# Optimization experiments

Measured on AMD Instinct MI355X. Metric: run time of the kernel, lower is better.

## Reference

```python
import jax, jax.numpy as jnp
import numpy as np

N, E, Z, H = 16384, 131072, 128, 8
ZH = Z // H
CUTOFF = 5.0


def _dense(key, din, dout, bias=True):
    kw, kb = jax.random.split(key)
    W = (jax.random.normal(kw, (din, dout), jnp.float32) / np.sqrt(din)).astype(jnp.float32)
    if bias:
        return W, jnp.zeros((dout,), jnp.float32)
    return W


def setup_inputs() -> dict:
    key = jax.random.key(0)
    ks = jax.random.split(key, 24)
    edge_index = jax.random.randint(ks[0], (2, E), 0, N)
    h_N_1_Z = jax.random.normal(ks[1], (N, 1, Z), jnp.float32)
    mu_N_L2_Z = jax.random.normal(ks[2], (N, 3, Z), jnp.float32) * 0.1
    ev = jax.random.normal(ks[3], (E, 3), jnp.float32)
    edge_vec_E_3 = ev / jnp.linalg.norm(ev, axis=-1, keepdims=True)
    edge_emb_E_Z = jax.random.normal(ks[4], (E, Z), jnp.float32)
    edge_weight_E = jax.random.uniform(ks[5], (E,), jnp.float32, 0.5, CUTOFF)
    deg = jax.ops.segment_sum(jnp.ones((E,), jnp.float32), edge_index[1], num_segments=N)
    num_edges_expanded_E = deg[edge_index[1]]
    inp = dict(edge_index=edge_index, h_N_1_Z=h_N_1_Z, mu_N_L2_Z=mu_N_L2_Z,
               edge_vec_E_3=edge_vec_E_3, edge_emb_E_Z=edge_emb_E_Z,
               edge_weight_E=edge_weight_E, num_edges_expanded_E=num_edges_expanded_E)
    inp['W_q'], inp['b_q'] = _dense(ks[6], Z, Z)
    inp['W_k'], inp['b_k'] = _dense(ks[7], Z, Z)
    inp['W_gs1'], inp['b_gs1'] = _dense(ks[8], Z, Z)
    inp['W_gs2'], inp['b_gs2'] = _dense(ks[9], Z, 3 * Z)
    inp['W_gv1'], inp['b_gv1'] = _dense(ks[10], Z, Z)
    inp['W_gv2'], inp['b_gv2'] = _dense(ks[11], Z, 3 * Z)
    inp['W_phik'], inp['b_phik'] = _dense(ks[12], Z, Z)
    inp['W_re'], inp['b_re'] = _dense(ks[13], Z, 3 * Z)
    inp['W_vq'] = _dense(ks[14], Z, Z, bias=False)   # vecq_w, no bias
    inp['W_vk0'] = _dense(ks[15], Z, Z, bias=False)  # veck_w[0] (lmax=1), no bias
    inp['W_lin'], inp['b_lin'] = _dense(ks[16], Z, Z)  # lin_w_linear
    inp['W_eu1'], inp['b_eu1'] = _dense(ks[17], Z, Z)  # edge_attr_up MLP [Z,Z,Z]
    inp['W_eu2'], inp['b_eu2'] = _dense(ks[18], Z, Z)
    return inp


def reference(edge_index, h_N_1_Z, mu_N_L2_Z, edge_vec_E_3, edge_emb_E_Z,
              edge_weight_E, num_edges_expanded_E,
              W_q, b_q, W_k, b_k, W_gs1, b_gs1, W_gs2, b_gs2,
              W_gv1, b_gv1, W_gv2, b_gv2, W_phik, b_phik, W_re, b_re,
              W_vq, W_vk0, W_lin, b_lin, W_eu1, b_eu1, W_eu2, b_eu2):
    silu = jax.nn.silu
    src, dst = edge_index[0], edge_index[1]  # messages j->i aggregated at dst=i
    hs = h_N_1_Z[:, 0]                        # (N, Z); layernorm='' -> identity
    q = (hs @ W_q + b_q).reshape(N, H, ZH)
    k = (hs @ W_k + b_k).reshape(N, H, ZH)
    x3 = silu(hs @ W_gs1 + b_gs1) @ W_gs2 + b_gs2    # gamma_s: (N, 3Z)
    val3 = silu(hs @ W_gv1 + b_gv1) @ W_gv2 + b_gv2  # gamma_v: (N, 3Z)
    r_attn = silu(edge_emb_E_Z @ W_phik + b_phik).reshape(E, H, ZH)
    r_ij = edge_emb_E_Z @ W_re + b_re                # (E, 3Z)

    # per-edge multi-head attention with segment softmax over target node
    logits = jnp.sum(q[dst] * k[src] * r_attn, axis=-1)        # (E, H)
    m = jax.ops.segment_max(logits, dst, num_segments=N)
    ex = jnp.exp(logits - m[dst])
    den = jax.ops.segment_sum(ex, dst, num_segments=N)
    attn = ex / den[dst]
    attn = attn * (jnp.sqrt(num_edges_expanded_E)[:, None] / np.float32(np.sqrt(Z)))

    sea = (attn[..., None] * val3[src].reshape(E, H, 3 * ZH)).reshape(E, 3 * Z)
    cut = 0.5 * (jnp.cos(jnp.pi * edge_weight_E / CUTOFF) + 1.0) * (edge_weight_E < CUTOFF)
    x_ij = cut[:, None] * sea * (x3[src] * r_ij)               # (E, 3Z)
    o_s, o_d, o_t = x_ij[:, :Z], x_ij[:, Z:2 * Z], x_ij[:, 2 * Z:]
    dmu_ij = o_d[:, None, :] * edge_vec_E_3[..., None] + o_t[:, None, :] * mu_N_L2_Z[src]  # (E,3,Z)

    h_out = h_N_1_Z + jax.ops.segment_sum(o_s, dst, num_segments=N)[:, None, :]
    mu_out = mu_N_L2_Z + jax.ops.segment_sum(dmu_ij, dst, num_segments=N)

    # edge update (sep_vecj, lmax=1 -> single degree block)
    w1 = jnp.einsum('nlz,ze->nle', mu_out, W_vq)
    w2 = jnp.einsum('nlz,ze->nle', mu_out, W_vk0)
    w1_d = jnp.sum(w1[dst] * edge_vec_E_3[..., None], axis=1)  # (E, evec)
    w2_d = jnp.sum(w2[src] * edge_vec_E_3[..., None], axis=1)
    w_dot = jnp.tanh((w1_d * w2_d) @ W_lin + b_lin)            # gated='gatedt'
    f_up = silu(edge_emb_E_Z @ W_eu1 + b_eu1) @ W_eu2 + b_eu2  # edge_attr_up MLP
    df_ij = edge_emb_E_Z + f_up * w_dot
    return h_out, mu_out, df_ij
```

## Files before the change

kernel.cpp:

```cpp
#include <hip/hip_runtime.h>
#include <math.h>

#define NN 16384
#define EE 131072
#define ZZ 128
#define HH 8

typedef short bf16x8 __attribute__((ext_vector_type(8)));
typedef float f32x4 __attribute__((ext_vector_type(4)));
typedef unsigned short ushort4v __attribute__((ext_vector_type(4)));
typedef unsigned short ushort8v __attribute__((ext_vector_type(8)));

__device__ __forceinline__ float silu_f(float x) { return x / (1.0f + __expf(-x)); }

__device__ __forceinline__ unsigned short f2bf(float x) {
    unsigned u = __float_as_uint(x);
    unsigned r = (u >> 16) & 1u;
    u += 0x7fffu + r;
    return (unsigned short)(u >> 16);
}
__device__ __forceinline__ float bf2f(unsigned short x) {
    return __uint_as_float(((unsigned)x) << 16);
}

__device__ __forceinline__ f32x4 mfma16(bf16x8 a, bf16x8 b, f32x4 c) {
    return __builtin_amdgcn_mfma_f32_16x16x32_bf16(a, b, c, 0, 0, 0);
}

__device__ __forceinline__ void stageB(const unsigned short* Wt, char* lB, int t) {
    const uint4* Wg = (const uint4*)Wt;
#pragma unroll
    for (int i = 0; i < 8; ++i) {
        const int cid = t + i * 256;
        const int n = cid >> 4, c16 = cid & 15;
        *(uint4*)(lB + ((n * 256 + c16 * 16) ^ ((n & 7) << 4))) = Wg[cid];
    }
}

struct WPrep {
    const float* w[13];
    int P[13];
    int tile0[14];
};

__global__ __launch_bounds__(128) void prep_weights(WPrep wp, unsigned short* wt) {
    int b = blockIdx.x, wi = 0;
    while (b >= wp.tile0[wi + 1]) ++wi;
    const int cg = (b - wp.tile0[wi]) * 128;
    const float* w = wp.w[wi];
    unsigned short* o = wt + (size_t)wp.tile0[wi] * 16384;
    const int P = wp.P[wi];
    const int t = threadIdx.x;
    for (int k0 = 0; k0 < 128; k0 += 8) {
        ushort8v v;
#pragma unroll
        for (int j = 0; j < 8; ++j) v[j] = f2bf(w[(size_t)(k0 + j) * P + cg + t]);
        *(ushort8v*)(o + (size_t)(cg + t) * 128 + k0) = v;
    }
}

struct BPrep {
    const float* b[13];
    int off[14];
};

__global__ __launch_bounds__(256) void prep_bias(BPrep bp, float* bcat) {
    const int idx = blockIdx.x * 256 + threadIdx.x;
    if (idx >= 2432) return;
    int wi = 0;
    while (idx >= bp.off[wi + 1]) ++wi;
    bcat[idx] = bp.b[wi] ? bp.b[wi][idx - bp.off[wi]] : 0.f;
}

__global__ __launch_bounds__(256) void prep_mub(const float* __restrict__ mu,
                                                unsigned short* __restrict__ mub) {
    const size_t idx = (size_t)blockIdx.x * 256 + threadIdx.x;
    const float4 a = ((const float4*)mu)[idx * 2];
    const float4 b = ((const float4*)mu)[idx * 2 + 1];
    ushort8v v;
    v[0] = f2bf(a.x); v[1] = f2bf(a.y); v[2] = f2bf(a.z); v[3] = f2bf(a.w);
    v[4] = f2bf(b.x); v[5] = f2bf(b.y); v[6] = f2bf(b.z); v[7] = f2bf(b.w);
    *(ushort8v*)(mub + idx * 8) = v;
}

template <int ACT, int INBF, int DUMP, int GATHERA>
__global__ __launch_bounds__(256, 2) void mm_bf16(
    const void* __restrict__ Av, const unsigned short* __restrict__ Wt,
    const float* __restrict__ bias, unsigned short* __restrict__ C,
    const unsigned short* __restrict__ aux, unsigned short* __restrict__ dumpA,
    const int* __restrict__ rowmap, int P, int As)
{
    __shared__ uint4 lA4[2048];
    __shared__ uint4 lB4[2048];
    char* lA = (char*)lA4;
    char* lB = (char*)lB4;
    const int t = threadIdx.x;
    const size_t row0 = (size_t)blockIdx.x * 128;
    const int cg = blockIdx.y * 128;
    if (INBF) {
        const uint4* Ag = (const uint4*)((const unsigned short*)Av + row0 * As);
        const int rs = As >> 3;
#pragma unroll
        for (int i = 0; i < 8; ++i) {
            const int chunk = t + i * 256;
            const int r = chunk >> 4, c16 = chunk & 15;
            *(uint4*)(lA + ((r * 256 + c16 * 16) ^ ((r & 7) << 4))) = Ag[r * rs + c16];
        }
    } else {
#pragma unroll
        for (int i = 0; i < 16; ++i) {
            const int f4 = t + i * 256;
            const int r = f4 >> 5, c4 = f4 & 31;
            const size_t gr = GATHERA ? (size_t)rowmap[row0 + r] : row0 + r;
            const float4 v = ((const float4*)((const float*)Av + gr * As))[c4];
            ushort4v bb;
            bb.x = f2bf(v.x); bb.y = f2bf(v.y); bb.z = f2bf(v.z); bb.w = f2bf(v.w);
            *(ushort4v*)(lA + ((r * 256 + c4 * 8) ^ ((r & 7) << 4))) = bb;
        }
    }
    stageB(Wt + (size_t)cg * 128, lB, t);
    __syncthreads();
    if (DUMP) {
#pragma unroll
        for (int i = 0; i < 8; ++i) {
            const int ch = t + i * 256;
            const int row = ch >> 4, cpos = ch & 15;
            const uint4 v = *(const uint4*)(lA + ((row * 256 + cpos * 16) ^ ((row & 7) << 4)));
            *(uint4*)(dumpA + (row0 + row) * 128 + cpos * 8) = v;
        }
    }
    const int lane = t & 63, wid = t >> 6;
    const int rbase = (wid >> 1) * 64, cbase = (wid & 1) * 64;
    const int lr = lane & 15, lgp = lane >> 4;
    f32x4 acc[4][4];
#pragma unroll
    for (int i = 0; i < 4; ++i)
#pragma unroll
        for (int j = 0; j < 4; ++j) acc[i][j] = (f32x4){0.f, 0.f, 0.f, 0.f};
#pragma unroll
    for (int ks = 0; ks < 4; ++ks) {
        bf16x8 av[4], bv[4];
#pragma unroll
        for (int mt = 0; mt < 4; ++mt) {
            const int r = rbase + mt * 16 + lr;
            av[mt] = *(const bf16x8*)(lA + ((r * 256 + ks * 64 + lgp * 16) ^ ((r & 7) << 4)));
        }
#pragma unroll
        for (int nt = 0; nt < 4; ++nt) {
            const int c = cbase + nt * 16 + lr;
            bv[nt] = *(const bf16x8*)(lB + ((c * 256 + ks * 64 + lgp * 16) ^ ((c & 7) << 4)));
        }
#pragma unroll
        for (int mt = 0; mt < 4; ++mt)
#pragma unroll
            for (int nt = 0; nt < 4; ++nt)
                acc[mt][nt] = mfma16(av[mt], bv[nt], acc[mt][nt]);
    }
    __syncthreads();
#pragma unroll
    for (int nt = 0; nt < 4; ++nt) {
        const int col = cbase + nt * 16 + lr;
        const int gcol = cg + col;
        const float b = bias[gcol];
#pragma unroll
        for (int mt = 0; mt < 4; ++mt) {
#pragma unroll
            for (int j = 0; j < 4; ++j) {
                const int row = rbase + mt * 16 + lgp * 4 + j;
                float v = acc[mt][nt][j] + b;
                if (ACT == 1) v = silu_f(v);
                if (ACT == 2) v = v * bf2f(aux[(row0 + row) * (size_t)P + gcol]);
                *(unsigned short*)(lB + ((row * 256 + col * 2) ^ ((row & 7) << 4))) = f2bf(v);
            }
        }
    }
    __syncthreads();
#pragma unroll
    for (int i = 0; i < 8; ++i) {
        const int ch = t + i * 256;
        const int row = ch >> 4, cpos = ch & 15;
        const uint4 v = *(const uint4*)(lB + ((row * 256 + cpos * 16) ^ ((row & 7) << 4)));
        *(uint4*)(C + (row0 + row) * (size_t)P + cg + cpos * 8) = v;
    }
}

__global__ __launch_bounds__(256, 3) void edge_mlp(
    const float* __restrict__ emb, const int* __restrict__ perm,
    const unsigned short* __restrict__ Wt1, const float* __restrict__ b1,
    const unsigned short* __restrict__ Wt2, const float* __restrict__ b2,
    unsigned short* __restrict__ embp, unsigned short* __restrict__ fup)
{
    __shared__ uint4 lA4[2048];
    char* lA = (char*)lA4;
    const int t = threadIdx.x;
    const size_t e0 = (size_t)blockIdx.x * 128;
#pragma unroll
    for (int i = 0; i < 16; ++i) {
        const int f4 = t + i * 256;
        const int r = f4 >> 5, c4 = f4 & 31;
        const size_t gr = (size_t)perm[e0 + r];
        const float4 v = ((const float4*)(emb + gr * 128))[c4];
        ushort4v bb;
        bb.x = f2bf(v.x); bb.y = f2bf(v.y); bb.z = f2bf(v.z); bb.w = f2bf(v.w);
        *(ushort4v*)(lA + ((r * 256 + c4 * 8) ^ ((r & 7) << 4))) = bb;
    }
    __syncthreads();
#pragma unroll
    for (int i = 0; i < 8; ++i) {
        const int ch = t + i * 256;
        const int row = ch >> 4, cpos = ch & 15;
        const uint4 v = *(const uint4*)(lA + ((row * 256 + cpos * 16) ^ ((row & 7) << 4)));
        *(uint4*)(embp + (e0 + row) * 128 + cpos * 8) = v;
    }
    const int lane = t & 63, wid = t >> 6;
    const int rbase = (wid >> 1) * 64, cbase = (wid & 1) * 64;
    const int lr = lane & 15, lgp = lane >> 4;
    f32x4 acc[4][4];
#pragma unroll
    for (int i = 0; i < 4; ++i)
#pragma unroll
        for (int j = 0; j < 4; ++j) acc[i][j] = (f32x4){0.f, 0.f, 0.f, 0.f};
#pragma unroll
    for (int ks = 0; ks < 4; ++ks) {
        bf16x8 av[4], bv[4];
#pragma unroll
        for (int mt = 0; mt < 4; ++mt) {
            const int r = rbase + mt * 16 + lr;
            av[mt] = *(const bf16x8*)(lA + ((r * 256 + ks * 64 + lgp * 16) ^ ((r & 7) << 4)));
        }
#pragma unroll
        for (int nt = 0; nt < 4; ++nt)
            bv[nt] = *(const bf16x8*)(Wt1 + (size_t)(cbase + nt * 16 + lr) * 128 + ks * 32 + lgp * 8);
#pragma unroll
        for (int mt = 0; mt < 4; ++mt)
#pragma unroll
            for (int nt = 0; nt < 4; ++nt)
                acc[mt][nt] = mfma16(bv[nt], av[mt], acc[mt][nt]);
    }
    __syncthreads();
#pragma unroll
    for (int mt = 0; mt < 4; ++mt) {
        const int row = rbase + mt * 16 + lr;
#pragma unroll
        for (int nt = 0; nt < 4; ++nt) {
            const int col = cbase + nt * 16 + lgp * 4;
            const float4 b4 = *(const float4*)(b1 + col);
            ushort4v st;
            st.x = f2bf(silu_f(acc[mt][nt][0] + b4.x));
            st.y = f2bf(silu_f(acc[mt][nt][1] + b4.y));
            st.z = f2bf(silu_f(acc[mt][nt][2] + b4.z));
            st.w = f2bf(silu_f(acc[mt][nt][3] + b4.w));
            *(ushort4v*)(lA + ((row * 256 + col * 2) ^ ((row & 7) << 4))) = st;
        }
    }
    __syncthreads();
#pragma unroll
    for (int i = 0; i < 4; ++i)
#pragma unroll
        for (int j = 0; j < 4; ++j) acc[i][j] = (f32x4){0.f, 0.f, 0.f, 0.f};
#pragma unroll
    for (int ks = 0; ks < 4; ++ks) {
        bf16x8 av[4], bv[4];
#pragma unroll
        for (int mt = 0; mt < 4; ++mt) {
            const int r = rbase + mt * 16 + lr;
            av[mt] = *(const bf16x8*)(lA + ((r * 256 + ks * 64 + lgp * 16) ^ ((r & 7) << 4)));
        }
#pragma unroll
        for (int nt = 0; nt < 4; ++nt)
            bv[nt] = *(const bf16x8*)(Wt2 + (size_t)(cbase + nt * 16 + lr) * 128 + ks * 32 + lgp * 8);
#pragma unroll
        for (int mt = 0; mt < 4; ++mt)
#pragma unroll
            for (int nt = 0; nt < 4; ++nt)
                acc[mt][nt] = mfma16(bv[nt], av[mt], acc[mt][nt]);
    }
    __syncthreads();
#pragma unroll
    for (int mt = 0; mt < 4; ++mt) {
        const int row = rbase + mt * 16 + lr;
#pragma unroll
        for (int nt = 0; nt < 4; ++nt) {
            const int col = cbase + nt * 16 + lgp * 4;
            const float4 b4 = *(const float4*)(b2 + col);
            ushort4v st;
            st.x = f2bf(acc[mt][nt][0] + b4.x);
            st.y = f2bf(acc[mt][nt][1] + b4.y);
            st.z = f2bf(acc[mt][nt][2] + b4.z);
            st.w = f2bf(acc[mt][nt][3] + b4.w);
            *(ushort4v*)(lA + ((row * 256 + col * 2) ^ ((row & 7) << 4))) = st;
        }
    }
    __syncthreads();
#pragma unroll
    for (int i = 0; i < 8; ++i) {
        const int ch = t + i * 256;
        const int row = ch >> 4, cpos = ch & 15;
        const uint4 v = *(const uint4*)(lA + ((row * 256 + cpos * 16) ^ ((row & 7) << 4)));
        *(uint4*)(fup + (e0 + row) * 128 + cpos * 8) = v;
    }
}

__global__ __launch_bounds__(256) void attn_kernel(
    const int* __restrict__ row_start, const int* __restrict__ srcp,
    const unsigned short* __restrict__ qkb, const unsigned short* __restrict__ rabp,
    const float* __restrict__ ewp, float* __restrict__ attnw)
{
    const int t = threadIdx.x;
    const int n = blockIdx.x * 4 + (t >> 6);
    const int lane = t & 63;
    const int el = lane >> 3, h = lane & 7;
    const int beg = row_start[n], end = row_start[n + 1];
    if (beg == end) return;
    const ushort8v q0 = *(const ushort8v*)(qkb + (size_t)n * 256 + h * 16);
    const ushort8v q1 = *(const ushort8v*)(qkb + (size_t)n * 256 + h * 16 + 8);
    float m = -1e30f, den = 0.f;
    for (int i0 = beg; i0 < end; i0 += 8) {
        const int i = i0 + el;
        const bool valid = i < end;
        const int ii = valid ? i : beg;
        const int s = srcp[ii];
        const ushort8v k0 = *(const ushort8v*)(qkb + (size_t)s * 256 + 128 + h * 16);
        const ushort8v k1 = *(const ushort8v*)(qkb + (size_t)s * 256 + 128 + h * 16 + 8);
        const ushort8v r0 = *(const ushort8v*)(rabp + (size_t)ii * 128 + h * 16);
        const ushort8v r1 = *(const ushort8v*)(rabp + (size_t)ii * 128 + h * 16 + 8);
        float lgv = 0.f;
#pragma unroll
        for (int j = 0; j < 8; ++j) lgv += bf2f(q0[j]) * bf2f(k0[j]) * bf2f(r0[j]);
#pragma unroll
        for (int j = 0; j < 8; ++j) lgv += bf2f(q1[j]) * bf2f(k1[j]) * bf2f(r1[j]);
        if (!valid) lgv = -1e30f;
        else attnw[(size_t)i * 8 + h] = lgv;
        float cm = lgv;
        cm = fmaxf(cm, __shfl_xor(cm, 8));
        cm = fmaxf(cm, __shfl_xor(cm, 16));
        cm = fmaxf(cm, __shfl_xor(cm, 32));
        const float nm = fmaxf(m, cm);
        float ex = valid ? __expf(lgv - nm) : 0.f;
        float cd = ex;
        cd += __shfl_xor(cd, 8);
        cd += __shfl_xor(cd, 16);
        cd += __shfl_xor(cd, 32);
        den = den * __expf(m - nm) + cd;
        m = nm;
    }
    const float sc = sqrtf((float)(end - beg)) * 0.08838834764831845f / den;
    for (int i0 = beg; i0 < end; i0 += 8) {
        const int i = i0 + el;
        if (i >= end) continue;
        const float w = ewp[i];
        const float cut = (w < 5.0f) ? 0.5f * (cosf(w * 0.62831853071795864f) + 1.0f) : 0.0f;
        const float lgv = attnw[(size_t)i * 8 + h];
        attnw[(size_t)i * 8 + h] = __expf(lgv - m) * sc * cut;
    }
}

__global__ __launch_bounds__(256, 3) void combine_mfma(
    const unsigned short* __restrict__ embp, const unsigned short* __restrict__ Wt_re,
    const float* __restrict__ bre, const float* __restrict__ attnw,
    unsigned short* __restrict__ ob)
{
    __shared__ uint4 lA4[2048];
    __shared__ float attnS[128 * 8];
    __shared__ uint4 scr4[512];
    char* lA = (char*)lA4;
    const int t = threadIdx.x;
    const size_t e0 = (size_t)blockIdx.x * 128;
    {
        const uint4* Ag = (const uint4*)(embp + e0 * 128);
#pragma unroll
        for (int i = 0; i < 8; ++i) {
            const int chunk = t + i * 256;
            const int r = chunk >> 4, c16 = chunk & 15;
            *(uint4*)(lA + ((r * 256 + c16 * 16) ^ ((r & 7) << 4))) = Ag[chunk];
        }
    }
    ((float4*)attnS)[t] = ((const float4*)(attnw + e0 * 8))[t];
    __syncthreads();
    const int lane = t & 63, wid = t >> 6;
    const int rbase = (wid >> 1) * 64, cbase = (wid & 1) * 64;
    const int lr = lane & 15, lgp = lane >> 4;
    char* swr = (char*)scr4 + wid * 2048;
    const int r2 = lane >> 3, c16r = lane & 7;
    for (int cg3 = 0; cg3 < 3; ++cg3) {
        const unsigned short* Wp = Wt_re + (size_t)cg3 * 16384;
        f32x4 acc[4][4];
#pragma unroll
        for (int i = 0; i < 4; ++i)
#pragma unroll
            for (int j = 0; j < 4; ++j) acc[i][j] = (f32x4){0.f, 0.f, 0.f, 0.f};
#pragma unroll
        for (int ks = 0; ks < 4; ++ks) {
            bf16x8 av[4], bv[4];
#pragma unroll
            for (int mt = 0; mt < 4; ++mt) {
                const int r = rbase + mt * 16 + lr;
                av[mt] = *(const bf16x8*)(lA + ((r * 256 + ks * 64 + lgp * 16) ^ ((r & 7) << 4)));
            }
#pragma unroll
            for (int nt = 0; nt < 4; ++nt)
                bv[nt] = *(const bf16x8*)(Wp + (size_t)(cbase + nt * 16 + lr) * 128 + ks * 32 + lgp * 8);
#pragma unroll
            for (int mt = 0; mt < 4; ++mt)
#pragma unroll
                for (int nt = 0; nt < 4; ++nt)
                    acc[mt][nt] = mfma16(bv[nt], av[mt], acc[mt][nt]);
        }
        const int cgo = cg3 * 128;
#pragma unroll
        for (int mt = 0; mt < 4; ++mt) {
            const int row = rbase + mt * 16 + lr;
            const float* aS = attnS + row * 8;
#pragma unroll
            for (int nt = 0; nt < 4; ++nt) {
                const int wc = nt * 16 + lgp * 4;
                const int gcol = cgo + cbase + wc;
                const float coef = aS[gcol / 48];
                const float4 b4 = *(const float4*)(bre + gcol);
                ushort4v st;
                st.x = f2bf((acc[mt][nt][0] + b4.x) * coef);
                st.y = f2bf((acc[mt][nt][1] + b4.y) * coef);
                st.z = f2bf((acc[mt][nt][2] + b4.z) * coef);
                st.w = f2bf((acc[mt][nt][3] + b4.w) * coef);
                *(ushort4v*)(swr + ((lr * 128 + wc * 2) ^ ((lr & 7) << 4))) = st;
            }
#pragma unroll
            for (int i = 0; i < 2; ++i) {
                const int rr = r2 + i * 8;
                const uint4 v = *(const uint4*)(swr + ((rr * 128 + c16r * 16) ^ ((rr & 7) << 4)));
                const size_t row_g = e0 + rbase + mt * 16 + rr;
                *(uint4*)(ob + row_g * 384 + cgo + cbase + c16r * 8) = v;
            }
        }
    }
}

__global__ __launch_bounds__(256, 3) void wdot_fused(
    const unsigned short* __restrict__ w12, const int* __restrict__ srcp,
    const int* __restrict__ dstp, const float* __restrict__ evp,
    const unsigned short* __restrict__ Wt_lin, const float* __restrict__ bl,
    const unsigned short* __restrict__ embp, const unsigned short* __restrict__ fup,
    const int* __restrict__ perm, float* __restrict__ df)
{
    __shared__ uint4 lA4[2048];
    char* lA = (char*)lA4;
    const int t = threadIdx.x;
    const size_t e0 = (size_t)blockIdx.x * 128;
#pragma unroll
    for (int i = 0; i < 8; ++i) {
        const int chunk = t + i * 256;
        const int r = chunk >> 4, c8 = chunk & 15;
        const size_t slot = e0 + r;
        const int s = srcp[slot], d = dstp[slot];
        const float e0v = evp[slot * 3 + 0], e1v = evp[slot * 3 + 1], e2v = evp[slot * 3 + 2];
        const ushort8v a0 = *(const ushort8v*)(w12 + ((size_t)d * 3 + 0) * 256 + c8 * 8);
        const ushort8v a1 = *(const ushort8v*)(w12 + ((size_t)d * 3 + 1) * 256 + c8 * 8);
        const ushort8v a2 = *(const ushort8v*)(w12 + ((size_t)d * 3 + 2) * 256 + c8 * 8);
        const ushort8v c0 = *(const ushort8v*)(w12 + ((size_t)s * 3 + 0) * 256 + 128 + c8 * 8);
        const ushort8v c1 = *(const ushort8v*)(w12 + ((size_t)s * 3 + 1) * 256 + 128 + c8 * 8);
        const ushort8v c2 = *(const ushort8v*)(w12 + ((size_t)s * 3 + 2) * 256 + 128 + c8 * 8);
        ushort8v o;
#pragma unroll
        for (int j = 0; j < 8; ++j) {
            const float av = e0v * bf2f(a0[j]) + e1v * bf2f(a1[j]) + e2v * bf2f(a2[j]);
            const float bv = e0v * bf2f(c0[j]) + e1v * bf2f(c1[j]) + e2v * bf2f(c2[j]);
            o[j] = f2bf(av * bv);
        }
        *(ushort8v*)(lA + ((r * 256 + c8 * 16) ^ ((r & 7) << 4))) = o;
    }
    __syncthreads();
    const int lane = t & 63, wid = t >> 6;
    const int rbase = (wid >> 1) * 64, cbase = (wid & 1) * 64;
    const int lr = lane & 15, lgp = lane >> 4;
    f32x4 acc[4][4];
#pragma unroll
    for (int i = 0; i < 4; ++i)
#pragma unroll
        for (int j = 0; j < 4; ++j) acc[i][j] = (f32x4){0.f, 0.f, 0.f, 0.f};
#pragma unroll
    for (int ks = 0; ks < 4; ++ks) {
        bf16x8 av[4], bv[4];
#pragma unroll
        for (int mt = 0; mt < 4; ++mt) {
            const int r = rbase + mt * 16 + lr;
            av[mt] = *(const bf16x8*)(lA + ((r * 256 + ks * 64 + lgp * 16) ^ ((r & 7) << 4)));
        }
#pragma unroll
        for (int nt = 0; nt < 4; ++nt)
            bv[nt] = *(const bf16x8*)(Wt_lin + (size_t)(cbase + nt * 16 + lr) * 128 + ks * 32 + lgp * 8);
#pragma unroll
        for (int mt = 0; mt < 4; ++mt)
#pragma unroll
            for (int nt = 0; nt < 4; ++nt)
                acc[mt][nt] = mfma16(bv[nt], av[mt], acc[mt][nt]);
    }
    __syncthreads();
    char* swr = lA + wid * 8192;
    const int r2 = lane >> 2, c4 = lane & 3;
#pragma unroll
    for (int mt = 0; mt < 4; ++mt) {
#pragma unroll
        for (int nt = 0; nt < 4; ++nt) {
            const int wc = nt * 16 + lgp * 4;
            const float4 b4 = *(const float4*)(bl + cbase + wc);
            float4 v;
            v.x = tanhf(acc[mt][nt][0] + b4.x);
            v.y = tanhf(acc[mt][nt][1] + b4.y);
            v.z = tanhf(acc[mt][nt][2] + b4.z);
            v.w = tanhf(acc[mt][nt][3] + b4.w);
            *(float4*)(swr + ((lr * 256 + wc * 4) ^ ((lr & 7) << 4))) = v;
        }
#pragma unroll
        for (int i = 0; i < 4; ++i) {
            const int chunk = i * 4 + c4;
            const float4 v = *(const float4*)(swr + ((r2 * 256 + chunk * 16) ^ ((r2 & 7) << 4)));
            const int row = rbase + mt * 16 + r2;
            const size_t sbase = (e0 + row) * 128 + cbase + chunk * 4;
            const ushort4v em = *(const ushort4v*)(embp + sbase);
            const ushort4v fu = *(const ushort4v*)(fup + sbase);
            const size_t orow = (size_t)perm[e0 + row];
            float4 o;
            o.x = bf2f(em.x) + bf2f(fu.x) * v.x;
            o.y = bf2f(em.y) + bf2f(fu.y) * v.y;
            o.z = bf2f(em.z) + bf2f(fu.z) * v.z;
            o.w = bf2f(em.w) + bf2f(fu.w) * v.w;
            *(float4*)(df + orow * 128 + cbase + chunk * 4) = o;
        }
    }
}

__global__ __launch_bounds__(256) void hist_kernel(const int* __restrict__ dst, int* __restrict__ counts) {
    const int e = blockIdx.x * 256 + threadIdx.x;
    atomicAdd(&counts[dst[e]], 1);
}

__global__ __launch_bounds__(256) void scan_kernel(const int* __restrict__ counts,
                                                   int* __restrict__ row_start,
                                                   int* __restrict__ cursor) {
    __shared__ int part[256];
    const int t = threadIdx.x;
    const int base = t * 64;
    int local[64];
    int s = 0;
#pragma unroll
    for (int i = 0; i < 64; ++i) { local[i] = s; s += counts[base + i]; }
    part[t] = s;
    __syncthreads();
    for (int off = 1; off < 256; off <<= 1) {
        int v = (t >= off) ? part[t - off] : 0;
        __syncthreads();
        part[t] += v;
        __syncthreads();
    }
    const int prev = (t == 0) ? 0 : part[t - 1];
#pragma unroll
    for (int i = 0; i < 64; ++i) {
        const int v = prev + local[i];
        row_start[base + i] = v;
        cursor[base + i] = v;
    }
    if (t == 255) row_start[NN] = prev + s;
}

__global__ __launch_bounds__(256) void fill_kernel(
    const int* __restrict__ src, const int* __restrict__ dst,
    const float* __restrict__ ewt, const float* __restrict__ ev,
    int* __restrict__ cursor, int* __restrict__ perm, int* __restrict__ srcp,
    int* __restrict__ dstp, float* __restrict__ ewp, float* __restrict__ evp)
{
    const int e = blockIdx.x * 256 + threadIdx.x;
    const int d = dst[e];
    const int p = atomicAdd(&cursor[d], 1);
    perm[p] = e;
    srcp[p] = src[e];
    dstp[p] = d;
    ewp[p] = ewt[e];
    evp[p * 3 + 0] = ev[e * 3 + 0];
    evp[p * 3 + 1] = ev[e * 3 + 1];
    evp[p * 3 + 2] = ev[e * 3 + 2];
}

__global__ __launch_bounds__(256) void gather_kernel(
    const int* __restrict__ row_start, const int* __restrict__ srcp,
    const unsigned short* __restrict__ ob, const unsigned short* __restrict__ xv,
    const unsigned short* __restrict__ mub, const float* __restrict__ evp,
    const float* __restrict__ h_in, const float* __restrict__ mu_in,
    float* __restrict__ h_out, float* __restrict__ mu_out)
{
    const int n = blockIdx.x * 4 + (threadIdx.x >> 6);
    const int t2 = (threadIdx.x & 63) * 2;
    const int beg = row_start[n], end = row_start[n + 1];
    float2 h2 = *(const float2*)(h_in + (size_t)n * 128 + t2);
    float2 m0 = *(const float2*)(mu_in + (size_t)n * 384 + t2);
    float2 m1 = *(const float2*)(mu_in + (size_t)n * 384 + 128 + t2);
    float2 m2 = *(const float2*)(mu_in + (size_t)n * 384 + 256 + t2);
#define GSTEP(i)  { \
        const int s = srcp[i]; \
        const float ev0 = evp[(i) * 3 + 0], ev1 = evp[(i) * 3 + 1], ev2 = evp[(i) * 3 + 2]; \
        const unsigned op0 = *(const unsigned*)(ob + (size_t)(i) * 384 + t2); \
        const unsigned op1 = *(const unsigned*)(ob + (size_t)(i) * 384 + 128 + t2); \
        const unsigned op2 = *(const unsigned*)(ob + (size_t)(i) * 384 + 256 + t2); \
        const unsigned xp0 = *(const unsigned*)(xv + (size_t)s * 384 + t2); \
        const unsigned xp1 = *(const unsigned*)(xv + (size_t)s * 384 + 128 + t2); \
        const unsigned xp2 = *(const unsigned*)(xv + (size_t)s * 384 + 256 + t2); \
        const unsigned mp0 = *(const unsigned*)(mub + (size_t)s * 384 + t2); \
        const unsigned mp1 = *(const unsigned*)(mub + (size_t)s * 384 + 128 + t2); \
        const unsigned mp2 = *(const unsigned*)(mub + (size_t)s * 384 + 256 + t2); \
        const float os0 = bf2f((unsigned short)op0) * bf2f((unsigned short)xp0); \
        const float os1 = bf2f((unsigned short)(op0 >> 16)) * bf2f((unsigned short)(xp0 >> 16)); \
        const float od0 = bf2f((unsigned short)op1) * bf2f((unsigned short)xp1); \
        const float od1 = bf2f((unsigned short)(op1 >> 16)) * bf2f((unsigned short)(xp1 >> 16)); \
        const float ot0 = bf2f((unsigned short)op2) * bf2f((unsigned short)xp2); \
        const float ot1 = bf2f((unsigned short)(op2 >> 16)) * bf2f((unsigned short)(xp2 >> 16)); \
        h2.x += os0; h2.y += os1; \
        m0.x += od0 * ev0 + ot0 * bf2f((unsigned short)mp0); \
        m0.y += od1 * ev0 + ot1 * bf2f((unsigned short)(mp0 >> 16)); \
        m1.x += od0 * ev1 + ot0 * bf2f((unsigned short)mp1); \
        m1.y += od1 * ev1 + ot1 * bf2f((unsigned short)(mp1 >> 16)); \
        m2.x += od0 * ev2 + ot0 * bf2f((unsigned short)mp2); \
        m2.y += od1 * ev2 + ot1 * bf2f((unsigned short)(mp2 >> 16)); \
    }
    int i = beg;
    for (; i + 1 < end; i += 2) { GSTEP(i); GSTEP(i + 1); }
    if (i < end) GSTEP(i);
#undef GSTEP
    *(float2*)(h_out + (size_t)n * 128 + t2) = h2;
    *(float2*)(mu_out + (size_t)n * 384 + t2) = m0;
    *(float2*)(mu_out + (size_t)n * 384 + 128 + t2) = m1;
    *(float2*)(mu_out + (size_t)n * 384 + 256 + t2) = m2;
}

extern "C" void kernel_launch(void* const* d_in, const int* in_sizes, int n_in,
                              void* d_out, int out_size, void* d_ws, size_t ws_size,
                              hipStream_t stream) {
    const int* eidx = (const int*)d_in[0];
    const int* src = eidx;
    const int* dst = eidx + EE;
    const float* h_in  = (const float*)d_in[1];
    const float* mu_in = (const float*)d_in[2];
    const float* ev    = (const float*)d_in[3];
    const float* emb   = (const float*)d_in[4];
    const float* ewt   = (const float*)d_in[5];
    const float* W_q   = (const float*)d_in[7];  const float* b_q   = (const float*)d_in[8];
    const float* W_k   = (const float*)d_in[9];  const float* b_k   = (const float*)d_in[10];
    const float* W_gs1 = (const float*)d_in[11]; const float* b_gs1 = (const float*)d_in[12];
    const float* W_gs2 = (const float*)d_in[13]; const float* b_gs2 = (const float*)d_in[14];
    const float* W_gv1 = (const float*)d_in[15]; const float* b_gv1 = (const float*)d_in[16];
    const float* W_gv2 = (const float*)d_in[17]; const float* b_gv2 = (const float*)d_in[18];
    const float* W_phik= (const float*)d_in[19]; const float* b_phik= (const float*)d_in[20];
    const float* W_re  = (const float*)d_in[21]; const float* b_re  = (const float*)d_in[22];
    const float* W_vq  = (const float*)d_in[23];
    const float* W_vk0 = (const float*)d_in[24];
    const float* W_lin = (const float*)d_in[25]; const float* b_lin = (const float*)d_in[26];
    const float* W_eu1 = (const float*)d_in[27]; const float* b_eu1 = (const float*)d_in[28];
    const float* W_eu2 = (const float*)d_in[29]; const float* b_eu2 = (const float*)d_in[30];

    float* out    = (float*)d_out;
    float* h_out  = out;
    float* mu_out = out + (size_t)NN * ZZ;
    float* df     = out + (size_t)NN * ZZ * 4;

    const size_t NZ = (size_t)NN * ZZ, N3Z = (size_t)NN * 3 * ZZ, EZ = (size_t)EE * ZZ;
    const size_t EH = (size_t)EE * HH;
    char* p = (char*)d_ws;
    unsigned short* qkb   = (unsigned short*)p; p += NZ * 2 * 2;
    unsigned short* tmpn2 = (unsigned short*)p; p += NZ * 2 * 2;
    unsigned short* x3b   = (unsigned short*)p; p += N3Z * 2;
    unsigned short* xv    = (unsigned short*)p; p += N3Z * 2;
    unsigned short* mub   = (unsigned short*)p; p += N3Z * 2;
    unsigned short* w12   = (unsigned short*)p; p += N3Z * 2 * 2;
    unsigned short* embp  = (unsigned short*)p; p += EZ * 2;
    unsigned short* rabp  = (unsigned short*)p; p += EZ * 2;
    unsigned short* fup   = (unsigned short*)p; p += EZ * 2;
    unsigned short* ob    = (unsigned short*)p; p += EZ * 3 * 2;
    float* attnw          = (float*)p;          p += EH * 4;
    unsigned short* wt    = (unsigned short*)p; p += 2432 * 128 * 2;
    float* bcat           = (float*)p;          p += 2432 * 4;
    int* counts           = (int*)p;            p += NN * 4;
    int* cursor           = (int*)p;            p += NN * 4;
    int* row_start        = (int*)p;            p += (NN + 1) * 4;
    int* perm             = (int*)p;            p += EE * 4;
    int* srcp             = (int*)p;            p += EE * 4;
    int* dstp             = (int*)p;            p += EE * 4;
    float* ewp            = (float*)p;          p += EE * 4;
    float* evp            = (float*)p;          p += EE * 12;

    const float* wsrc[13] = {W_q, W_k, W_gs1, W_gv1, W_gs2, W_gv2, W_phik,
                             W_re, W_vq, W_vk0, W_lin, W_eu1, W_eu2};
    const float* bsrc[13] = {b_q, b_k, b_gs1, b_gv1, b_gs2, b_gv2, b_phik,
                             b_re, nullptr, nullptr, b_lin, b_eu1, b_eu2};
    const int Ps[13] = {128, 128, 128, 128, 384, 384, 128, 384, 128, 128, 128, 128, 128};
    WPrep wp; BPrep bp;
    int tiles = 0;
    for (int i = 0; i < 13; ++i) {
        wp.w[i] = wsrc[i]; wp.P[i] = Ps[i]; wp.tile0[i] = tiles;
        bp.b[i] = bsrc[i]; bp.off[i] = tiles * 128;
        tiles += Ps[i] / 128;
    }
    wp.tile0[13] = tiles; bp.off[13] = tiles * 128;
    unsigned short* wT[13]; const float* bC[13];
    for (int i = 0; i < 13; ++i) { wT[i] = wt + (size_t)wp.tile0[i] * 16384; bC[i] = bcat + bp.off[i]; }

    dim3 blk(256);
    prep_weights<<<dim3(tiles), dim3(128), 0, stream>>>(wp, wt);
    prep_bias<<<dim3(10), blk, 0, stream>>>(bp, bcat);
    prep_mub<<<dim3(N3Z / 8 / 256), blk, 0, stream>>>(mu_in, mub);
    hipMemsetAsync(counts, 0, NN * 4, stream);
    hist_kernel<<<dim3(EE/256), blk, 0, stream>>>(dst, counts);
    scan_kernel<<<dim3(1), blk, 0, stream>>>(counts, row_start, cursor);
    fill_kernel<<<dim3(EE/256), blk, 0, stream>>>(src, dst, ewt, ev, cursor, perm, srcp, dstp, ewp, evp);
    mm_bf16<0,0,0,0><<<dim3(NN/128, 2), blk, 0, stream>>>(h_in, wT[0], bC[0], qkb, nullptr, nullptr, nullptr, 256, 128);
    mm_bf16<1,0,0,0><<<dim3(NN/128, 2), blk, 0, stream>>>(h_in, wT[2], bC[2], tmpn2, nullptr, nullptr, nullptr, 256, 128);
    mm_bf16<0,1,0,0><<<dim3(NN/128, 3), blk, 0, stream>>>(tmpn2, wT[4], bC[4], x3b, nullptr, nullptr, nullptr, 384, 256);
    mm_bf16<2,1,0,0><<<dim3(NN/128, 3), blk, 0, stream>>>(tmpn2 + 128, wT[5], bC[5], xv, x3b, nullptr, nullptr, 384, 256);
    edge_mlp<<<dim3(EE/128), blk, 0, stream>>>(emb, perm, wT[11], bC[11], wT[12], bC[12], embp, fup);
    mm_bf16<1,1,0,0><<<dim3(EE/128, 1), blk, 0, stream>>>(embp, wT[6], bC[6], rabp, nullptr, nullptr, nullptr, 128, 128);
    attn_kernel<<<dim3(NN/4), blk, 0, stream>>>(row_start, srcp, qkb, rabp, ewp, attnw);
    combine_mfma<<<dim3(EE/128), blk, 0, stream>>>(embp, wT[7], bC[7], attnw, ob);
    gather_kernel<<<dim3(NN/4), blk, 0, stream>>>(
        row_start, srcp, ob, xv, mub, evp, h_in, mu_in, h_out, mu_out);
    mm_bf16<0,0,0,0><<<dim3(3*NN/128, 2), blk, 0, stream>>>(mu_out, wT[8], bC[8], w12, nullptr, nullptr, nullptr, 256, 128);
    wdot_fused<<<dim3(EE/128), blk, 0, stream>>>(
        w12, srcp, dstp, evp, wT[10], bC[10], embp, fup, perm, df);
}
```

Measured before the change: 386.6 us.

## Fuse phik edge GEMM into edge_mlp and read embp directly in combine

The separate mm_bf16 launch that computed silu(emb@W_phik+b) into rabp is folded into edge_mlp, reusing the emb tile already in LDS. Epilogues in edge_mlp now stage each warp's 16-row slab through a small per-warp scratch, which drops block-wide barriers. combine_mfma no longer stages embp into LDS and loads A fragments straight from global memory, and its occupancy hint is raised from 3 to 5. The goal is to save one kernel launch, one read of embp and some LDS and sync overhead. The cost is more per-block work in edge_mlp and uncoalesced global A loads in combine.

```diff
diff --git a/kernel.cpp b/kernel.cpp
--- a/kernel.cpp
+++ b/kernel.cpp
@@ -186,11 +186,14 @@
 
 __global__ __launch_bounds__(256, 3) void edge_mlp(
     const float* __restrict__ emb, const int* __restrict__ perm,
+    const unsigned short* __restrict__ Wt_phik, const float* __restrict__ b_phik,
     const unsigned short* __restrict__ Wt1, const float* __restrict__ b1,
     const unsigned short* __restrict__ Wt2, const float* __restrict__ b2,
-    unsigned short* __restrict__ embp, unsigned short* __restrict__ fup)
+    unsigned short* __restrict__ embp, unsigned short* __restrict__ rabp,
+    unsigned short* __restrict__ fup)
 {
     __shared__ uint4 lA4[2048];
+    __shared__ uint4 scr4[512];
     char* lA = (char*)lA4;
     const int t = threadIdx.x;
     const size_t e0 = (size_t)blockIdx.x * 128;
@@ -215,7 +218,51 @@
     const int lane = t & 63, wid = t >> 6;
     const int rbase = (wid >> 1) * 64, cbase = (wid & 1) * 64;
     const int lr = lane & 15, lgp = lane >> 4;
+    char* swr = (char*)scr4 + wid * 2048;
+    const int r2 = lane >> 3, c16r = lane & 7;
     f32x4 acc[4][4];
+#pragma unroll
+    for (int i = 0; i < 4; ++i)
+#pragma unroll
+        for (int j = 0; j < 4; ++j) acc[i][j] = (f32x4){0.f, 0.f, 0.f, 0.f};
+#pragma unroll
+    for (int ks = 0; ks < 4; ++ks) {
+        bf16x8 av[4], bv[4];
+#pragma unroll
+        for (int mt = 0; mt < 4; ++mt) {
+            const int r = rbase + mt * 16 + lr;
+            av[mt] = *(const bf16x8*)(lA + ((r * 256 + ks * 64 + lgp * 16) ^ ((r & 7) << 4)));
+        }
+#pragma unroll
+        for (int nt = 0; nt < 4; ++nt)
+            bv[nt] = *(const bf16x8*)(Wt_phik + (size_t)(cbase + nt * 16 + lr) * 128 + ks * 32 + lgp * 8);
+#pragma unroll
+        for (int mt = 0; mt < 4; ++mt)
+#pragma unroll
+            for (int nt = 0; nt < 4; ++nt)
+                acc[mt][nt] = mfma16(bv[nt], av[mt], acc[mt][nt]);
+    }
+#pragma unroll
+    for (int mt = 0; mt < 4; ++mt) {
+#pragma unroll
+        for (int nt = 0; nt < 4; ++nt) {
+            const int wc = nt * 16 + lgp * 4;
+            const float4 b4 = *(const float4*)(b_phik + cbase + wc);
+            ushort4v st;
+            st.x = f2bf(silu_f(acc[mt][nt][0] + b4.x));
+            st.y = f2bf(silu_f(acc[mt][nt][1] + b4.y));
+            st.z = f2bf(silu_f(acc[mt][nt][2] + b4.z));
+            st.w = f2bf(silu_f(acc[mt][nt][3] + b4.w));
+            *(ushort4v*)(swr + ((lr * 128 + wc * 2) ^ ((lr & 7) << 4))) = st;
+        }
+#pragma unroll
+        for (int i = 0; i < 2; ++i) {
+            const int rr = r2 + i * 8;
+            const uint4 v = *(const uint4*)(swr + ((rr * 128 + c16r * 16) ^ ((rr & 7) << 4)));
+            const size_t row_g = e0 + rbase + mt * 16 + rr;
+            *(uint4*)(rabp + row_g * 128 + cbase + c16r * 8) = v;
+        }
+    }
 #pragma unroll
     for (int i = 0; i < 4; ++i)
 #pragma unroll
@@ -275,29 +322,26 @@
             for (int nt = 0; nt < 4; ++nt)
                 acc[mt][nt] = mfma16(bv[nt], av[mt], acc[mt][nt]);
     }
-    __syncthreads();
 #pragma unroll
     for (int mt = 0; mt < 4; ++mt) {
-        const int row = rbase + mt * 16 + lr;
 #pragma unroll
         for (int nt = 0; nt < 4; ++nt) {
-            const int col = cbase + nt * 16 + lgp * 4;
-            const float4 b4 = *(const float4*)(b2 + col);
+            const int wc = nt * 16 + lgp * 4;
+            const float4 b4 = *(const float4*)(b2 + cbase + wc);
             ushort4v st;
             st.x = f2bf(acc[mt][nt][0] + b4.x);
             st.y = f2bf(acc[mt][nt][1] + b4.y);
             st.z = f2bf(acc[mt][nt][2] + b4.z);
             st.w = f2bf(acc[mt][nt][3] + b4.w);
-            *(ushort4v*)(lA + ((row * 256 + col * 2) ^ ((row & 7) << 4))) = st;
-        }
-    }
-    __syncthreads();
-#pragma unroll
-    for (int i = 0; i < 8; ++i) {
-        const int ch = t + i * 256;
-        const int row = ch >> 4, cpos = ch & 15;
-        const uint4 v = *(const uint4*)(lA + ((row * 256 + cpos * 16) ^ ((row & 7) << 4)));
-        *(uint4*)(fup + (e0 + row) * 128 + cpos * 8) = v;
+            *(ushort4v*)(swr + ((lr * 128 + wc * 2) ^ ((lr & 7) << 4))) = st;
+        }
+#pragma unroll
+        for (int i = 0; i < 2; ++i) {
+            const int rr = r2 + i * 8;
+            const uint4 v = *(const uint4*)(swr + ((rr * 128 + c16r * 16) ^ ((rr & 7) << 4)));
+            const size_t row_g = e0 + rbase + mt * 16 + rr;
+            *(uint4*)(fup + row_g * 128 + cbase + c16r * 8) = v;
+        }
     }
 }
 
@@ -355,26 +399,15 @@
     }
 }
 
-__global__ __launch_bounds__(256, 3) void combine_mfma(
+__global__ __launch_bounds__(256, 5) void combine_mfma(
     const unsigned short* __restrict__ embp, const unsigned short* __restrict__ Wt_re,
     const float* __restrict__ bre, const float* __restrict__ attnw,
     unsigned short* __restrict__ ob)
 {
-    __shared__ uint4 lA4[2048];
     __shared__ float attnS[128 * 8];
     __shared__ uint4 scr4[512];
-    char* lA = (char*)lA4;
     const int t = threadIdx.x;
     const size_t e0 = (size_t)blockIdx.x * 128;
-    {
-        const uint4* Ag = (const uint4*)(embp + e0 * 128);
-#pragma unroll
-        for (int i = 0; i < 8; ++i) {
-            const int chunk = t + i * 256;
-            const int r = chunk >> 4, c16 = chunk & 15;
-            *(uint4*)(lA + ((r * 256 + c16 * 16) ^ ((r & 7) << 4))) = Ag[chunk];
-        }
-    }
     ((float4*)attnS)[t] = ((const float4*)(attnw + e0 * 8))[t];
     __syncthreads();
     const int lane = t & 63, wid = t >> 6;
@@ -393,10 +426,8 @@
         for (int ks = 0; ks < 4; ++ks) {
             bf16x8 av[4], bv[4];
 #pragma unroll
-            for (int mt = 0; mt < 4; ++mt) {
-                const int r = rbase + mt * 16 + lr;
-                av[mt] = *(const bf16x8*)(lA + ((r * 256 + ks * 64 + lgp * 16) ^ ((r & 7) << 4)));
-            }
+            for (int mt = 0; mt < 4; ++mt)
+                av[mt] = *(const bf16x8*)(embp + (e0 + rbase + mt * 16 + lr) * 128 + ks * 32 + lgp * 8);
 #pragma unroll
             for (int nt = 0; nt < 4; ++nt)
                 bv[nt] = *(const bf16x8*)(Wp + (size_t)(cbase + nt * 16 + lr) * 128 + ks * 32 + lgp * 8);
@@ -713,8 +744,8 @@
     mm_bf16<1,0,0,0><<<dim3(NN/128, 2), blk, 0, stream>>>(h_in, wT[2], bC[2], tmpn2, nullptr, nullptr, nullptr, 256, 128);
     mm_bf16<0,1,0,0><<<dim3(NN/128, 3), blk, 0, stream>>>(tmpn2, wT[4], bC[4], x3b, nullptr, nullptr, nullptr, 384, 256);
     mm_bf16<2,1,0,0><<<dim3(NN/128, 3), blk, 0, stream>>>(tmpn2 + 128, wT[5], bC[5], xv, x3b, nullptr, nullptr, 384, 256);
-    edge_mlp<<<dim3(EE/128), blk, 0, stream>>>(emb, perm, wT[11], bC[11], wT[12], bC[12], embp, fup);
-    mm_bf16<1,1,0,0><<<dim3(EE/128, 1), blk, 0, stream>>>(embp, wT[6], bC[6], rabp, nullptr, nullptr, nullptr, 128, 128);
+    edge_mlp<<<dim3(EE/128), blk, 0, stream>>>(
+        emb, perm, wT[6], bC[6], wT[11], bC[11], wT[12], bC[12], embp, rabp, fup);
     attn_kernel<<<dim3(NN/4), blk, 0, stream>>>(row_start, srcp, qkb, rabp, ewp, attnw);
     combine_mfma<<<dim3(EE/128), blk, 0, stream>>>(embp, wT[7], bC[7], attnw, ob);
     gather_kernel<<<dim3(NN/4), blk, 0, stream>>>(
```

Result: slower. 445.3 us (+15.2%).
